# Kernel optimization log

Measured on AMD Instinct MI355X. Metric: run time of the kernel, lower is better.

The kernel has to match this reference:

```python
import jax, jax.numpy as jnp
import numpy as np

DRUG_DIM, PROT_DIM, HIDDEN_DIM, OUTPUT_DIM = 128, 128, 256, 256


def setup_inputs() -> dict:
    key = jax.random.key(0)
    ks = jax.random.split(key, 7)
    B, n_d, n_p = 8, 64, 1024
    s = lambda d: 1.0 / np.sqrt(d)
    return {
        "X_d": jax.random.normal(ks[0], (B, n_d, DRUG_DIM), dtype=jnp.float32),
        "X_p": jax.random.normal(ks[1], (B, n_p, PROT_DIM), dtype=jnp.float32),
        # nn.Linear(in, out) weights have shape (out, in); we store transposed (in, out)
        "W_d": jax.random.uniform(ks[2], (DRUG_DIM, HIDDEN_DIM), jnp.float32, -s(DRUG_DIM), s(DRUG_DIM)),
        "W_p": jax.random.uniform(ks[3], (PROT_DIM, HIDDEN_DIM), jnp.float32, -s(PROT_DIM), s(PROT_DIM)),
        "W_a": jax.random.uniform(ks[4], (DRUG_DIM, OUTPUT_DIM), jnp.float32, -s(DRUG_DIM), s(DRUG_DIM)),
        "W_b": jax.random.uniform(ks[5], (PROT_DIM, OUTPUT_DIM), jnp.float32, -s(PROT_DIM), s(PROT_DIM)),
        "w_score": jax.random.uniform(ks[6], (HIDDEN_DIM,), jnp.float32, -s(HIDDEN_DIM), s(HIDDEN_DIM)),
    }


def reference(X_d, X_p, W_d, W_p, W_a, W_b, w_score):
    # Projections: (B, n_d, H), (B, n_p, H), (B, n_d, O), (B, n_p, O)
    hd = jnp.einsum("bik,kh->bih", X_d, W_d)
    hp = jnp.einsum("bjk,kh->bjh", X_p, W_p)
    fd = jnp.einsum("bik,ko->bio", X_d, W_a)
    fp = jnp.einsum("bjk,ko->bjo", X_p, W_b)

    # N_ij = tanh(hd_i + hp_j): (B, n_d, n_p, H); scores = N @ w_score
    N = jnp.tanh(hd[:, :, None, :] + hp[:, None, :, :])
    scores = jnp.einsum("bijh,h->bij", N, w_score)
    A = jax.nn.softmax(scores, axis=-1)  # softmax over protein dim

    # f_ij = tanh(fd_i + fp_j): (B, n_d, n_p, O)
    f = jnp.tanh(fd[:, :, None, :] + fp[:, None, :, :])
    X_int = jnp.einsum("bij,bijo->bo", A, f)  # sum over i and j
    return X_int
```

## Files before the change

kernel.cpp:

```cpp
#include <hip/hip_runtime.h>

#define NB   8
#define ND   64
#define NP   1024
#define KDIM 128
#define HID  256
#define OUTD 256
#define CSC  2.885390081777927f

typedef __attribute__((ext_vector_type(8))) short  bf16x8;
typedef __attribute__((ext_vector_type(4))) float  f32x4;


__device__ __forceinline__ ushort f2bf(float f) {
    unsigned u = __float_as_uint(f);
    unsigned r = (u + 0x7FFFu + ((u >> 16) & 1u)) >> 16;
    return (ushort)r;
}

__global__ __launch_bounds__(256) void k_cast(
    const float* __restrict__ Xd, const float* __restrict__ Xp,
    const float* __restrict__ Wd, const float* __restrict__ Wa,
    const float* __restrict__ Wp, const float* __restrict__ Wb,
    ushort* __restrict__ Xdbf, ushort* __restrict__ Xpbf,
    ushort* __restrict__ WdT, ushort* __restrict__ WaT,
    ushort* __restrict__ WpT, ushort* __restrict__ WbT) {
    int blk = blockIdx.x, t = threadIdx.x;
    if (blk < 1024) {
        size_t i = ((size_t)blk << 10) + ((size_t)t << 2);
        float4 v = *(const float4*)(Xp + i);
        ushort4 o; o.x = f2bf(v.x); o.y = f2bf(v.y); o.z = f2bf(v.z); o.w = f2bf(v.w);
        *(ushort4*)(Xpbf + i) = o;
    } else if (blk < 1088) {
        size_t i = ((size_t)(blk - 1024) << 10) + ((size_t)t << 2);
        float4 v = *(const float4*)(Xd + i);
        ushort4 o; o.x = f2bf(v.x); o.y = f2bf(v.y); o.z = f2bf(v.z); o.w = f2bf(v.w);
        *(ushort4*)(Xdbf + i) = o;
    } else {
        int r = blk - 1088, mat = r >> 5;
        const float* W = (mat == 0) ? Wd : (mat == 1) ? Wa : (mat == 2) ? Wp : Wb;
        ushort* WT = (mat == 0) ? WdT : (mat == 1) ? WaT : (mat == 2) ? WpT : WbT;
        int o0 = ((r & 31) << 10) + (t << 2);
        int n = o0 >> 7, k0 = o0 & 127;
        ushort4 o;
        o.x = f2bf(W[(k0 + 0) * HID + n]);
        o.y = f2bf(W[(k0 + 1) * HID + n]);
        o.z = f2bf(W[(k0 + 2) * HID + n]);
        o.w = f2bf(W[(k0 + 3) * HID + n]);
        *(ushort4*)(WT + o0) = o;
    }
}

__global__ __launch_bounds__(256) void k_proj_mfma(
    const ushort* __restrict__ Xpbf, const ushort* __restrict__ Xdbf,
    const ushort* __restrict__ WdT, const ushort* __restrict__ WaT,
    const ushort* __restrict__ WpT, const ushort* __restrict__ WbT,
    float* __restrict__ Ehd, float* __restrict__ Efd,
    float* __restrict__ EhpT, float* __restrict__ Efp) {
    int blk = blockIdx.x, t = threadIdx.x;
    const ushort *A, *B;
    float* out; size_t obase; int ostride, am0, bn0;
    if (blk < 512) {
        int mt = blk >> 2, nt = blk & 3;
        A = Xpbf; am0 = mt * 64; B = WbT; bn0 = nt * 64;
        out = Efp; obase = (size_t)am0 * HID + bn0; ostride = HID;
    } else if (blk < 1024) {
        int r = blk - 512, b = r >> 6, rr = r & 63;
        int mt = rr >> 4, nt = rr & 15;
        A = WpT; am0 = mt * 64;
        B = Xpbf + (size_t)b * NP * KDIM; bn0 = nt * 64;
        out = EhpT; obase = ((size_t)(b * 256 + am0)) * NP + bn0; ostride = NP;
    } else if (blk < 1056) {
        int r = blk - 1024; int mt = r >> 2, nt = r & 3;
        A = Xdbf; am0 = mt * 64; B = WdT; bn0 = nt * 64;
        out = Ehd; obase = (size_t)am0 * HID + bn0; ostride = HID;
    } else {
        int r = blk - 1056; int mt = r >> 2, nt = r & 3;
        A = Xdbf; am0 = mt * 64; B = WaT; bn0 = nt * 64;
        out = Efd; obase = (size_t)am0 * HID + bn0; ostride = HID;
    }
    int l = t & 63, w = t >> 6;
    int wm = (w >> 1) << 5, wn = (w & 1) << 5;
    int lr = l & 15, lk = (l >> 4) << 3;
    const ushort* Ab = A + (size_t)(am0 + wm + lr) * KDIM + lk;
    const ushort* Bb = B + (size_t)(bn0 + wn + lr) * KDIM + lk;

    bf16x8 af[2][4], bf[2][4];
#pragma unroll
    for (int f = 0; f < 2; ++f)
#pragma unroll
        for (int ks = 0; ks < 4; ++ks) {
            af[f][ks] = *(const bf16x8*)(Ab + (size_t)(f << 4) * KDIM + (ks << 5));
            bf[f][ks] = *(const bf16x8*)(Bb + (size_t)(f << 4) * KDIM + (ks << 5));
        }

    f32x4 acc[2][2];
#pragma unroll
    for (int mf = 0; mf < 2; ++mf)
#pragma unroll
        for (int nf = 0; nf < 2; ++nf) acc[mf][nf] = (f32x4){0.f, 0.f, 0.f, 0.f};
#pragma unroll
    for (int ks = 0; ks < 4; ++ks)
#pragma unroll
        for (int mf = 0; mf < 2; ++mf)
#pragma unroll
            for (int nf = 0; nf < 2; ++nf)
                acc[mf][nf] = __builtin_amdgcn_mfma_f32_16x16x32_bf16(
                    af[mf][ks], bf[nf][ks], acc[mf][nf], 0, 0, 0);

#pragma unroll
    for (int mf = 0; mf < 2; ++mf)
#pragma unroll
        for (int nf = 0; nf < 2; ++nf)
#pragma unroll
            for (int r = 0; r < 4; ++r) {
                int m = wm + (mf << 4) + ((l >> 4) << 2) + r;
                int n = wn + (nf << 4) + (l & 15);
                out[obase + (size_t)m * ostride + n] =
                    __builtin_amdgcn_exp2f(acc[mf][nf][r] * CSC);
            }
}

__global__ __launch_bounds__(256) void k_scores(
    const float* __restrict__ Ehd, const float* __restrict__ EhpT,
    const float* __restrict__ wsc, float* __restrict__ S) {
    int blk = blockIdx.x;
    int b = blk >> 7, r = blk & 127, it = r >> 4, jt = r & 15;
    int i0 = it * 8, j0 = jt * 64;
    int t = threadIdx.x;
    int jg = t & 63, iq = t >> 6;
    int i = i0 + iq * 2;
    const float4* h0v4 = (const float4*)(Ehd + ((b * ND + i) << 8));
    const float4* h1v4 = (const float4*)(Ehd + ((b * ND + i + 1) << 8));
    const float4* w4   = (const float4*)wsc;
    const float* pT = EhpT + ((size_t)(b << 8)) * NP + j0 + jg;
    float acc0 = 0.f, acc1 = 0.f;
#pragma unroll 4
    for (int h4 = 0; h4 < 64; ++h4) {
        float4 h0 = h0v4[h4];
        float4 h1 = h1v4[h4];
        float4 wv = w4[h4];
        float p0 = pT[(h4 * 4 + 0) * NP];
        float p1 = pT[(h4 * 4 + 1) * NP];
        float p2 = pT[(h4 * 4 + 2) * NP];
        float p3 = pT[(h4 * 4 + 3) * NP];
        acc0 = fmaf(wv.x, __builtin_amdgcn_rcpf(fmaf(h0.x, p0, 1.f)), acc0);
        acc0 = fmaf(wv.y, __builtin_amdgcn_rcpf(fmaf(h0.y, p1, 1.f)), acc0);
        acc0 = fmaf(wv.z, __builtin_amdgcn_rcpf(fmaf(h0.z, p2, 1.f)), acc0);
        acc0 = fmaf(wv.w, __builtin_amdgcn_rcpf(fmaf(h0.w, p3, 1.f)), acc0);
        acc1 = fmaf(wv.x, __builtin_amdgcn_rcpf(fmaf(h1.x, p0, 1.f)), acc1);
        acc1 = fmaf(wv.y, __builtin_amdgcn_rcpf(fmaf(h1.y, p1, 1.f)), acc1);
        acc1 = fmaf(wv.z, __builtin_amdgcn_rcpf(fmaf(h1.z, p2, 1.f)), acc1);
        acc1 = fmaf(wv.w, __builtin_amdgcn_rcpf(fmaf(h1.w, p3, 1.f)), acc1);
    }
    int base = ((b * ND + i) << 10) + j0 + jg;
    S[base]        = -2.f * acc0;
    S[base + 1024] = -2.f * acc1;
}

__global__ __launch_bounds__(256) void k_softmax(float* __restrict__ S) {
    int row = blockIdx.x;
    int t = threadIdx.x;
    float* Srow = S + (row << 10);
    float4 v = ((float4*)Srow)[t];
    const float L2E = 1.4426950408889634f;
    v.x = __builtin_amdgcn_exp2f(v.x * L2E);
    v.y = __builtin_amdgcn_exp2f(v.y * L2E);
    v.z = __builtin_amdgcn_exp2f(v.z * L2E);
    v.w = __builtin_amdgcn_exp2f(v.w * L2E);
    float s4 = (v.x + v.y) + (v.z + v.w);
#pragma unroll
    for (int off = 32; off > 0; off >>= 1) s4 += __shfl_xor(s4, off, 64);
    __shared__ float wsum[4];
    if ((t & 63) == 0) wsum[t >> 6] = s4;
    __syncthreads();
    float tot = (wsum[0] + wsum[1]) + (wsum[2] + wsum[3]);
    float sneg = -2.0f * __builtin_amdgcn_rcpf(tot);
    v.x *= sneg; v.y *= sneg; v.z *= sneg; v.w *= sneg;
    ((float4*)Srow)[t] = v;
}

__global__ __launch_bounds__(256) void k_facc(
    const float* __restrict__ Efd, const float* __restrict__ Efp,
    const float* __restrict__ A2, float* __restrict__ part) {
    int blk = blockIdx.x;
    int b = blk >> 7, rr = blk & 127, ih = rr >> 6, jt = rr & 63;
    int i0 = ih * 32, j0 = jt * 16;
    int t = threadIdx.x;
    __shared__ float4 as4[32 * 4];
    __shared__ float4 red[256];
    if (t < 128) {
        int ii = t >> 2, jq = t & 3;
        as4[t] = ((const float4*)A2)[((b * ND + i0 + ii) << 8) + (j0 >> 2) + jq];
    }
    __syncthreads();

    int o4 = t & 63, jq = t >> 6;
    const float4* fdg = (const float4*)(Efd + ((b * ND + i0) << 8));
    const float4* fpg = (const float4*)(Efp + ((b * NP + j0 + (jq << 2)) << 8));
    float4 fv0 = fpg[o4], fv1 = fpg[64 + o4], fv2 = fpg[128 + o4], fv3 = fpg[192 + o4];
    float4 acc = {0.f, 0.f, 0.f, 0.f};
    for (int i = 0; i < 32; ++i) {
        float4 dv = fdg[(i << 6) + o4];
        float4 a  = as4[(i << 2) + jq];
        acc.x = fmaf(a.x, __builtin_amdgcn_rcpf(fmaf(dv.x, fv0.x, 1.f)), acc.x);
        acc.y = fmaf(a.x, __builtin_amdgcn_rcpf(fmaf(dv.y, fv0.y, 1.f)), acc.y);
        acc.z = fmaf(a.x, __builtin_amdgcn_rcpf(fmaf(dv.z, fv0.z, 1.f)), acc.z);
        acc.w = fmaf(a.x, __builtin_amdgcn_rcpf(fmaf(dv.w, fv0.w, 1.f)), acc.w);
        acc.x = fmaf(a.y, __builtin_amdgcn_rcpf(fmaf(dv.x, fv1.x, 1.f)), acc.x);
        acc.y = fmaf(a.y, __builtin_amdgcn_rcpf(fmaf(dv.y, fv1.y, 1.f)), acc.y);
        acc.z = fmaf(a.y, __builtin_amdgcn_rcpf(fmaf(dv.z, fv1.z, 1.f)), acc.z);
        acc.w = fmaf(a.y, __builtin_amdgcn_rcpf(fmaf(dv.w, fv1.w, 1.f)), acc.w);
        acc.x = fmaf(a.z, __builtin_amdgcn_rcpf(fmaf(dv.x, fv2.x, 1.f)), acc.x);
        acc.y = fmaf(a.z, __builtin_amdgcn_rcpf(fmaf(dv.y, fv2.y, 1.f)), acc.y);
        acc.z = fmaf(a.z, __builtin_amdgcn_rcpf(fmaf(dv.z, fv2.z, 1.f)), acc.z);
        acc.w = fmaf(a.z, __builtin_amdgcn_rcpf(fmaf(dv.w, fv2.w, 1.f)), acc.w);
        acc.x = fmaf(a.w, __builtin_amdgcn_rcpf(fmaf(dv.x, fv3.x, 1.f)), acc.x);
        acc.y = fmaf(a.w, __builtin_amdgcn_rcpf(fmaf(dv.y, fv3.y, 1.f)), acc.y);
        acc.z = fmaf(a.w, __builtin_amdgcn_rcpf(fmaf(dv.z, fv3.z, 1.f)), acc.z);
        acc.w = fmaf(a.w, __builtin_amdgcn_rcpf(fmaf(dv.w, fv3.w, 1.f)), acc.w);
    }
    red[t] = acc; __syncthreads();
    if (t < 64) {
        float4 r0 = red[t], r1 = red[64 + t], r2 = red[128 + t], r3 = red[192 + t];
        float4 s;
        s.x = (r0.x + r1.x) + (r2.x + r3.x);
        s.y = (r0.y + r1.y) + (r2.y + r3.y);
        s.z = (r0.z + r1.z) + (r2.z + r3.z);
        s.w = (r0.w + r1.w) + (r2.w + r3.w);
        ((float4*)part)[(blk << 6) + t] = s;
    }
}

__global__ __launch_bounds__(256) void k_reduce(
    const float* __restrict__ part, float* __restrict__ out) {
    int b = blockIdx.x >> 3, oc = blockIdx.x & 7;
    int t = threadIdx.x;
    int o = oc * 32 + (t & 31), q0 = t >> 5;
    float s = 0.f;
#pragma unroll
    for (int k = 0; k < 16; ++k)
        s += part[((b * 128 + q0 + k * 8) << 8) + o];
    __shared__ float red[256];
    red[t] = s; __syncthreads();
    for (int st = 128; st >= 32; st >>= 1) {
        if (t < st) red[t] += red[t + st];
        __syncthreads();
    }
    if (t < 32) out[(b << 8) + oc * 32 + t] = 64.0f + red[t];
}

extern "C" void kernel_launch(void* const* d_in, const int* in_sizes, int n_in,
                              void* d_out, int out_size, void* d_ws, size_t ws_size,
                              hipStream_t stream) {
    const float* Xd  = (const float*)d_in[0];
    const float* Xp  = (const float*)d_in[1];
    const float* Wd  = (const float*)d_in[2];
    const float* Wp  = (const float*)d_in[3];
    const float* Wa  = (const float*)d_in[4];
    const float* Wb  = (const float*)d_in[5];
    const float* wsc = (const float*)d_in[6];
    float* out = (float*)d_out;

    float* ws = (float*)d_ws;
    float* Ehd  = ws;
    float* Efd  = Ehd + NB * ND * HID;
    float* EhpT = Efd + NB * ND * OUTD;
    float* Efp  = EhpT + NB * NP * HID;
    float* S    = Efp + NB * NP * OUTD;
    ushort* Xpbf = (ushort*)S;
    ushort* Xdbf = (ushort*)(S + NB * ND * NP);
    ushort* WdT  = Xdbf + 65536;
    ushort* WaT  = WdT + 32768;
    ushort* WpT  = WaT + 32768;
    ushort* WbT  = WpT + 32768;
    float* part  = EhpT;

    k_cast     <<<1216, 256, 0, stream>>>(Xd, Xp, Wd, Wa, Wp, Wb,
                                          Xdbf, Xpbf, WdT, WaT, WpT, WbT);
    k_proj_mfma<<<1088, 256, 0, stream>>>(Xpbf, Xdbf, WdT, WaT, WpT, WbT,
                                          Ehd, Efd, EhpT, Efp);
    k_scores   <<<1024, 256, 0, stream>>>(Ehd, EhpT, wsc, S);
    k_softmax  <<<NB * ND, 256, 0, stream>>>(S);
    k_facc     <<<NB * 128, 256, 0, stream>>>(Efd, Efp, S, part);
    k_reduce   <<<64, 256, 0, stream>>>(part, out);
}
```

Baseline: 72.38 us.

## Fuse scores, softmax and weighted tanh accumulation into one per-row kernel

Merges the score, softmax and f-accumulation kernels into a single 512-thread block per (batch, drug row). Each block computes the full 1024-wide score row in registers, does the softmax with a block reduction, keeps the attention weights in shared memory, and accumulates over all proteins for all 256 outputs. The final reduce shrinks to 8 blocks summing 64 partials each. This removes the global round-trip of the score matrix and two launches. In exchange the grid drops to 512 blocks, and the f-stage reads the whole Efp per drug row rather than reusing it across 32 rows.

```diff
diff --git a/kernel.cpp b/kernel.cpp
--- a/kernel.cpp
+++ b/kernel.cpp
@@ -14,8 +14,7 @@
 
 __device__ __forceinline__ ushort f2bf(float f) {
     unsigned u = __float_as_uint(f);
-    unsigned r = (u + 0x7FFFu + ((u >> 16) & 1u)) >> 16;
-    return (ushort)r;
+    return (ushort)((u + 0x7FFFu + ((u >> 16) & 1u)) >> 16);
 }
 
 __global__ __launch_bounds__(256) void k_cast(
@@ -85,13 +84,13 @@
     const ushort* Ab = A + (size_t)(am0 + wm + lr) * KDIM + lk;
     const ushort* Bb = B + (size_t)(bn0 + wn + lr) * KDIM + lk;
 
-    bf16x8 af[2][4], bf[2][4];
+    bf16x8 af[2][4], bfr[2][4];
 #pragma unroll
     for (int f = 0; f < 2; ++f)
 #pragma unroll
         for (int ks = 0; ks < 4; ++ks) {
-            af[f][ks] = *(const bf16x8*)(Ab + (size_t)(f << 4) * KDIM + (ks << 5));
-            bf[f][ks] = *(const bf16x8*)(Bb + (size_t)(f << 4) * KDIM + (ks << 5));
+            af[f][ks]  = *(const bf16x8*)(Ab + (size_t)(f << 4) * KDIM + (ks << 5));
+            bfr[f][ks] = *(const bf16x8*)(Bb + (size_t)(f << 4) * KDIM + (ks << 5));
         }
 
     f32x4 acc[2][2];
@@ -106,7 +105,7 @@
 #pragma unroll
             for (int nf = 0; nf < 2; ++nf)
                 acc[mf][nf] = __builtin_amdgcn_mfma_f32_16x16x32_bf16(
-                    af[mf][ks], bf[nf][ks], acc[mf][nf], 0, 0, 0);
+                    af[mf][ks], bfr[nf][ks], acc[mf][nf], 0, 0, 0);
 
 #pragma unroll
     for (int mf = 0; mf < 2; ++mf)
@@ -121,133 +120,92 @@
             }
 }
 
-__global__ __launch_bounds__(256) void k_scores(
+__global__ __launch_bounds__(512) void k_fused(
     const float* __restrict__ Ehd, const float* __restrict__ EhpT,
-    const float* __restrict__ wsc, float* __restrict__ S) {
+    const float* __restrict__ Efd, const float* __restrict__ Efp,
+    const float* __restrict__ wsc, float* __restrict__ part) {
     int blk = blockIdx.x;
-    int b = blk >> 7, r = blk & 127, it = r >> 4, jt = r & 15;
-    int i0 = it * 8, j0 = jt * 64;
+    int b = blk >> 6;
     int t = threadIdx.x;
-    int jg = t & 63, iq = t >> 6;
-    int i = i0 + iq * 2;
-    const float4* h0v4 = (const float4*)(Ehd + ((b * ND + i) << 8));
-    const float4* h1v4 = (const float4*)(Ehd + ((b * ND + i + 1) << 8));
-    const float4* w4   = (const float4*)wsc;
-    const float* pT = EhpT + ((size_t)(b << 8)) * NP + j0 + jg;
+    __shared__ float4 hs4[64];
+    __shared__ float4 w24[64];
+    __shared__ float4 a2v[256];
+    __shared__ float  red[512];
+    if (t < 64) {
+        hs4[t] = ((const float4*)(Ehd + ((size_t)blk << 8)))[t];
+        float4 wv = ((const float4*)wsc)[t];
+        w24[t] = make_float4(-2.f * wv.x, -2.f * wv.y, -2.f * wv.z, -2.f * wv.w);
+    }
+    __syncthreads();
+
+    const float* pT = EhpT + ((size_t)(b << 8)) * NP + t;
     float acc0 = 0.f, acc1 = 0.f;
-#pragma unroll 4
     for (int h4 = 0; h4 < 64; ++h4) {
-        float4 h0 = h0v4[h4];
-        float4 h1 = h1v4[h4];
-        float4 wv = w4[h4];
-        float p0 = pT[(h4 * 4 + 0) * NP];
-        float p1 = pT[(h4 * 4 + 1) * NP];
-        float p2 = pT[(h4 * 4 + 2) * NP];
-        float p3 = pT[(h4 * 4 + 3) * NP];
-        acc0 = fmaf(wv.x, __builtin_amdgcn_rcpf(fmaf(h0.x, p0, 1.f)), acc0);
-        acc0 = fmaf(wv.y, __builtin_amdgcn_rcpf(fmaf(h0.y, p1, 1.f)), acc0);
-        acc0 = fmaf(wv.z, __builtin_amdgcn_rcpf(fmaf(h0.z, p2, 1.f)), acc0);
-        acc0 = fmaf(wv.w, __builtin_amdgcn_rcpf(fmaf(h0.w, p3, 1.f)), acc0);
-        acc1 = fmaf(wv.x, __builtin_amdgcn_rcpf(fmaf(h1.x, p0, 1.f)), acc1);
-        acc1 = fmaf(wv.y, __builtin_amdgcn_rcpf(fmaf(h1.y, p1, 1.f)), acc1);
-        acc1 = fmaf(wv.z, __builtin_amdgcn_rcpf(fmaf(h1.z, p2, 1.f)), acc1);
-        acc1 = fmaf(wv.w, __builtin_amdgcn_rcpf(fmaf(h1.w, p3, 1.f)), acc1);
-    }
-    int base = ((b * ND + i) << 10) + j0 + jg;
-    S[base]        = -2.f * acc0;
-    S[base + 1024] = -2.f * acc1;
-}
-
-__global__ __launch_bounds__(256) void k_softmax(float* __restrict__ S) {
-    int row = blockIdx.x;
-    int t = threadIdx.x;
-    float* Srow = S + (row << 10);
-    float4 v = ((float4*)Srow)[t];
+        float4 hv = hs4[h4];
+        float4 wv = w24[h4];
+        const float* pb = pT + (size_t)(h4 << 2) * NP;
+        float p0 = pb[0],        q0 = pb[512];
+        float p1 = pb[NP],       q1 = pb[NP + 512];
+        float p2 = pb[2 * NP],   q2 = pb[2 * NP + 512];
+        float p3 = pb[3 * NP],   q3 = pb[3 * NP + 512];
+        acc0 = fmaf(wv.x, __builtin_amdgcn_rcpf(fmaf(hv.x, p0, 1.f)), acc0);
+        acc1 = fmaf(wv.x, __builtin_amdgcn_rcpf(fmaf(hv.x, q0, 1.f)), acc1);
+        acc0 = fmaf(wv.y, __builtin_amdgcn_rcpf(fmaf(hv.y, p1, 1.f)), acc0);
+        acc1 = fmaf(wv.y, __builtin_amdgcn_rcpf(fmaf(hv.y, q1, 1.f)), acc1);
+        acc0 = fmaf(wv.z, __builtin_amdgcn_rcpf(fmaf(hv.z, p2, 1.f)), acc0);
+        acc1 = fmaf(wv.z, __builtin_amdgcn_rcpf(fmaf(hv.z, q2, 1.f)), acc1);
+        acc0 = fmaf(wv.w, __builtin_amdgcn_rcpf(fmaf(hv.w, p3, 1.f)), acc0);
+        acc1 = fmaf(wv.w, __builtin_amdgcn_rcpf(fmaf(hv.w, q3, 1.f)), acc1);
+    }
+
     const float L2E = 1.4426950408889634f;
-    v.x = __builtin_amdgcn_exp2f(v.x * L2E);
-    v.y = __builtin_amdgcn_exp2f(v.y * L2E);
-    v.z = __builtin_amdgcn_exp2f(v.z * L2E);
-    v.w = __builtin_amdgcn_exp2f(v.w * L2E);
-    float s4 = (v.x + v.y) + (v.z + v.w);
+    float e0 = __builtin_amdgcn_exp2f(acc0 * L2E);
+    float e1 = __builtin_amdgcn_exp2f(acc1 * L2E);
+    float s4 = e0 + e1;
 #pragma unroll
     for (int off = 32; off > 0; off >>= 1) s4 += __shfl_xor(s4, off, 64);
-    __shared__ float wsum[4];
+    __shared__ float wsum[8];
     if ((t & 63) == 0) wsum[t >> 6] = s4;
     __syncthreads();
-    float tot = (wsum[0] + wsum[1]) + (wsum[2] + wsum[3]);
+    float tot = ((wsum[0] + wsum[1]) + (wsum[2] + wsum[3])) +
+                ((wsum[4] + wsum[5]) + (wsum[6] + wsum[7]));
     float sneg = -2.0f * __builtin_amdgcn_rcpf(tot);
-    v.x *= sneg; v.y *= sneg; v.z *= sneg; v.w *= sneg;
-    ((float4*)Srow)[t] = v;
-}
-
-__global__ __launch_bounds__(256) void k_facc(
-    const float* __restrict__ Efd, const float* __restrict__ Efp,
-    const float* __restrict__ A2, float* __restrict__ part) {
-    int blk = blockIdx.x;
-    int b = blk >> 7, rr = blk & 127, ih = rr >> 6, jt = rr & 63;
-    int i0 = ih * 32, j0 = jt * 16;
-    int t = threadIdx.x;
-    __shared__ float4 as4[32 * 4];
-    __shared__ float4 red[256];
-    if (t < 128) {
-        int ii = t >> 2, jq = t & 3;
-        as4[t] = ((const float4*)A2)[((b * ND + i0 + ii) << 8) + (j0 >> 2) + jq];
-    }
-    __syncthreads();
-
-    int o4 = t & 63, jq = t >> 6;
-    const float4* fdg = (const float4*)(Efd + ((b * ND + i0) << 8));
-    const float4* fpg = (const float4*)(Efp + ((b * NP + j0 + (jq << 2)) << 8));
-    float4 fv0 = fpg[o4], fv1 = fpg[64 + o4], fv2 = fpg[128 + o4], fv3 = fpg[192 + o4];
-    float4 acc = {0.f, 0.f, 0.f, 0.f};
-    for (int i = 0; i < 32; ++i) {
-        float4 dv = fdg[(i << 6) + o4];
-        float4 a  = as4[(i << 2) + jq];
-        acc.x = fmaf(a.x, __builtin_amdgcn_rcpf(fmaf(dv.x, fv0.x, 1.f)), acc.x);
-        acc.y = fmaf(a.x, __builtin_amdgcn_rcpf(fmaf(dv.y, fv0.y, 1.f)), acc.y);
-        acc.z = fmaf(a.x, __builtin_amdgcn_rcpf(fmaf(dv.z, fv0.z, 1.f)), acc.z);
-        acc.w = fmaf(a.x, __builtin_amdgcn_rcpf(fmaf(dv.w, fv0.w, 1.f)), acc.w);
-        acc.x = fmaf(a.y, __builtin_amdgcn_rcpf(fmaf(dv.x, fv1.x, 1.f)), acc.x);
-        acc.y = fmaf(a.y, __builtin_amdgcn_rcpf(fmaf(dv.y, fv1.y, 1.f)), acc.y);
-        acc.z = fmaf(a.y, __builtin_amdgcn_rcpf(fmaf(dv.z, fv1.z, 1.f)), acc.z);
-        acc.w = fmaf(a.y, __builtin_amdgcn_rcpf(fmaf(dv.w, fv1.w, 1.f)), acc.w);
-        acc.x = fmaf(a.z, __builtin_amdgcn_rcpf(fmaf(dv.x, fv2.x, 1.f)), acc.x);
-        acc.y = fmaf(a.z, __builtin_amdgcn_rcpf(fmaf(dv.y, fv2.y, 1.f)), acc.y);
-        acc.z = fmaf(a.z, __builtin_amdgcn_rcpf(fmaf(dv.z, fv2.z, 1.f)), acc.z);
-        acc.w = fmaf(a.z, __builtin_amdgcn_rcpf(fmaf(dv.w, fv2.w, 1.f)), acc.w);
-        acc.x = fmaf(a.w, __builtin_amdgcn_rcpf(fmaf(dv.x, fv3.x, 1.f)), acc.x);
-        acc.y = fmaf(a.w, __builtin_amdgcn_rcpf(fmaf(dv.y, fv3.y, 1.f)), acc.y);
-        acc.z = fmaf(a.w, __builtin_amdgcn_rcpf(fmaf(dv.z, fv3.z, 1.f)), acc.z);
-        acc.w = fmaf(a.w, __builtin_amdgcn_rcpf(fmaf(dv.w, fv3.w, 1.f)), acc.w);
-    }
-    red[t] = acc; __syncthreads();
-    if (t < 64) {
-        float4 r0 = red[t], r1 = red[64 + t], r2 = red[128 + t], r3 = red[192 + t];
-        float4 s;
-        s.x = (r0.x + r1.x) + (r2.x + r3.x);
-        s.y = (r0.y + r1.y) + (r2.y + r3.y);
-        s.z = (r0.z + r1.z) + (r2.z + r3.z);
-        s.w = (r0.w + r1.w) + (r2.w + r3.w);
-        ((float4*)part)[(blk << 6) + t] = s;
-    }
+    float* a2 = (float*)a2v;
+    a2[t]       = e0 * sneg;
+    a2[t + 512] = e1 * sneg;
+    __syncthreads();
+
+    int o = t & 255, half = t >> 8;
+    float fdv = Efd[((size_t)blk << 8) + o];
+    const float* fp = Efp + (((size_t)(b * NP + (half << 9))) << 8) + o;
+    const float4* ah = a2v + (half << 7);
+    float accA = 0.f, accB = 0.f;
+    for (int j4 = 0; j4 < 128; ++j4) {
+        const float* fj = fp + ((size_t)j4 << 10);
+        float f0 = fj[0];
+        float f1 = fj[256];
+        float f2 = fj[512];
+        float f3 = fj[768];
+        float4 av = ah[j4];
+        accA = fmaf(av.x, __builtin_amdgcn_rcpf(fmaf(fdv, f0, 1.f)), accA);
+        accB = fmaf(av.y, __builtin_amdgcn_rcpf(fmaf(fdv, f1, 1.f)), accB);
+        accA = fmaf(av.z, __builtin_amdgcn_rcpf(fmaf(fdv, f2, 1.f)), accA);
+        accB = fmaf(av.w, __builtin_amdgcn_rcpf(fmaf(fdv, f3, 1.f)), accB);
+    }
+    red[t] = accA + accB;
+    __syncthreads();
+    if (t < 256)
+        part[((size_t)blk << 8) + t] = red[t] + red[t + 256];
 }
 
 __global__ __launch_bounds__(256) void k_reduce(
     const float* __restrict__ part, float* __restrict__ out) {
-    int b = blockIdx.x >> 3, oc = blockIdx.x & 7;
-    int t = threadIdx.x;
-    int o = oc * 32 + (t & 31), q0 = t >> 5;
-    float s = 0.f;
-#pragma unroll
-    for (int k = 0; k < 16; ++k)
-        s += part[((b * 128 + q0 + k * 8) << 8) + o];
-    __shared__ float red[256];
-    red[t] = s; __syncthreads();
-    for (int st = 128; st >= 32; st >>= 1) {
-        if (t < st) red[t] += red[t + st];
-        __syncthreads();
-    }
-    if (t < 32) out[(b << 8) + oc * 32 + t] = 64.0f + red[t];
+    int b = blockIdx.x, t = threadIdx.x;
+    float s = 64.0f;
+#pragma unroll 8
+    for (int i = 0; i < 64; ++i)
+        s += part[((size_t)(b * 64 + i) << 8) + t];
+    out[(b << 8) + t] = s;
 }
 
 extern "C" void kernel_launch(void* const* d_in, const int* in_sizes, int n_in,
@@ -267,21 +225,19 @@
     float* Efd  = Ehd + NB * ND * HID;
     float* EhpT = Efd + NB * ND * OUTD;
     float* Efp  = EhpT + NB * NP * HID;
-    float* S    = Efp + NB * NP * OUTD;
-    ushort* Xpbf = (ushort*)S;
-    ushort* Xdbf = (ushort*)(S + NB * ND * NP);
+    float* stage = Efp + NB * NP * OUTD;
+    ushort* Xpbf = (ushort*)stage;
+    ushort* Xdbf = Xpbf + NB * NP * KDIM;
     ushort* WdT  = Xdbf + 65536;
     ushort* WaT  = WdT + 32768;
     ushort* WpT  = WaT + 32768;
     ushort* WbT  = WpT + 32768;
-    float* part  = EhpT;
+    float* part  = stage;
 
     k_cast     <<<1216, 256, 0, stream>>>(Xd, Xp, Wd, Wa, Wp, Wb,
                                           Xdbf, Xpbf, WdT, WaT, WpT, WbT);
     k_proj_mfma<<<1088, 256, 0, stream>>>(Xpbf, Xdbf, WdT, WaT, WpT, WbT,
                                           Ehd, Efd, EhpT, Efp);
-    k_scores   <<<1024, 256, 0, stream>>>(Ehd, EhpT, wsc, S);
-    k_softmax  <<<NB * ND, 256, 0, stream>>>(S);
-    k_facc     <<<NB * 128, 256, 0, stream>>>(Efd, Efp, S, part);
-    k_reduce   <<<64, 256, 0, stream>>>(part, out);
-}
+    k_fused    <<<NB * ND, 512, 0, stream>>>(Ehd, EhpT, Efd, Efp, wsc, part);
+    k_reduce   <<<NB, 256, 0, stream>>>(part, out);
+}
```

Result: no change. 71.74 us (-0.9%).
